# Kernel optimization log

Measured on AMD Instinct MI355X. Metric: run time of the kernel, lower is better.

The kernel has to match this reference:

```python
import jax, jax.numpy as jnp
import numpy as np

EMBED_DIM = 1024
N_HEADS = 16
KV_SIZE = 64
CLIP_DIST = 10
SLEN = 1024
BSZ = 8


def setup_inputs() -> dict:
    key = jax.random.key(0)
    ks = jax.random.split(key, 7)
    s = 0.02
    inputs = jax.random.normal(ks[0], (SLEN, BSZ, EMBED_DIM), dtype=jnp.float32)
    W_in = jax.random.normal(ks[1], (3 * N_HEADS * KV_SIZE, EMBED_DIM), dtype=jnp.float32) * s
    b_in = jnp.zeros((3 * N_HEADS * KV_SIZE,), dtype=jnp.float32)
    k_dist_emb = jax.random.normal(ks[2], (CLIP_DIST + 1, KV_SIZE), dtype=jnp.float32) * s
    v_dist_emb = jax.random.normal(ks[3], (CLIP_DIST + 1, KV_SIZE), dtype=jnp.float32) * s
    W_out = jax.random.normal(ks[4], (EMBED_DIM, N_HEADS * KV_SIZE), dtype=jnp.float32) * s
    b_out = jnp.zeros((EMBED_DIM,), dtype=jnp.float32)
    return {"inputs": inputs, "W_in": W_in, "b_in": b_in,
            "k_dist_emb": k_dist_emb, "v_dist_emb": v_dist_emb,
            "W_out": W_out, "b_out": b_out}


def reference(inputs, W_in, b_in, k_dist_emb, v_dist_emb, W_out, b_out):
    slen, bsz, _ = inputs.shape
    h, d = N_HEADS, KV_SIZE
    # in_proj: (slen, bsz, 3*h*d) -> (3, bsz, h, slen, d)
    qkv = inputs @ W_in.T + b_in
    qkv = qkv.reshape(slen, bsz, 3, h, d).transpose(2, 1, 3, 0, 4)
    q, k, v = qkv[0], qkv[1], qkv[2]
    q = q * (d ** -0.5)
    # clipped absolute relative distances (slen, slen)
    idx = jnp.arange(slen)
    dist = jnp.minimum(jnp.abs(idx[None, :] - idx[:, None]), CLIP_DIST)
    k_dist = k_dist_emb[dist]  # (slen, slen, d)
    v_dist = v_dist_emb[dist]  # (slen, slen, d)
    # content scores + relative-distance bias
    attn = jnp.einsum('bhsd,bhtd->bhst', q, k) + jnp.einsum('bhsd,std->bhst', q, k_dist)
    attn = jax.nn.softmax(attn, axis=-1)
    # value accumulation + relative-distance value correction
    out = jnp.einsum('bhst,bhtd->bhsd', attn, v) + jnp.einsum('bhst,std->bhsd', attn, v_dist)
    # (bsz, h, slen, d) -> (slen, bsz, h*d)
    out = out.transpose(2, 0, 1, 3).reshape(slen, bsz, h * d)
    return out @ W_out.T + b_out
```

## Files before the change

kernel.cpp:

```cpp
#include <hip/hip_runtime.h>
#include <hip/hip_bf16.h>
#include <cstdint>


typedef __attribute__((ext_vector_type(8))) __bf16 bf16x8;
typedef __attribute__((ext_vector_type(4))) __bf16 bf16x4;
typedef __attribute__((ext_vector_type(4))) short s16x4;
typedef __attribute__((ext_vector_type(4))) float f32x4;

#if __has_builtin(__builtin_amdgcn_exp2f)
#define EXP2F(x) __builtin_amdgcn_exp2f(x)
#else
#define EXP2F(x) exp2f(x)
#endif

#if __has_builtin(__builtin_amdgcn_mfma_f32_16x16x16bf16_1k)
#define PV_MFMA(ACC, AV, BV) \
  ACC = __builtin_amdgcn_mfma_f32_16x16x16bf16_1k( \
      __builtin_bit_cast(s16x4, AV), __builtin_bit_cast(s16x4, BV), ACC, 0, 0, 0)
#elif __has_builtin(__builtin_amdgcn_mfma_f32_16x16x16_bf16)
#define PV_MFMA(ACC, AV, BV) \
  ACC = __builtin_amdgcn_mfma_f32_16x16x16_bf16(AV, BV, ACC, 0, 0, 0)
#else
#define PV_MFMA(ACC, AV, BV)                                               \
  asm volatile("s_nop 1\n\tv_mfma_f32_16x16x16_bf16 %0, %1, %2, %0\n\t"    \
               "s_nop 7\n\ts_nop 7"                                        \
               : "+v"(ACC)                                                 \
               : "v"(__builtin_bit_cast(s16x4, AV)),                       \
                 "v"(__builtin_bit_cast(s16x4, BV)))
#endif

__device__ __forceinline__ void gload_lds16(const void* g, void* l) {
  __builtin_amdgcn_global_load_lds(
      (const __attribute__((address_space(1))) void*)g,
      (__attribute__((address_space(3))) void*)l, 16, 0, 0);
}

__global__ __launch_bounds__(256) void f2b3_kernel(
    const float* __restrict__ s0, __bf16* __restrict__ d0,
    const float* __restrict__ s1, __bf16* __restrict__ d1,
    const float* __restrict__ s2, __bf16* __restrict__ d2) {
  int i = (blockIdx.x * 256 + threadIdx.x) * 8;
  const float* s; __bf16* d; int off;
  if (i < 8388608) { s = s0; d = d0; off = i; }
  else if (i < 11534336) { s = s1; d = d1; off = i - 8388608; }
  else { s = s2; d = d2; off = i - 11534336; }
  float4 a = *(const float4*)(s + off);
  float4 b = *(const float4*)(s + off + 4);
  bf16x8 o;
  o[0] = (__bf16)a.x; o[1] = (__bf16)a.y; o[2] = (__bf16)a.z; o[3] = (__bf16)a.w;
  o[4] = (__bf16)b.x; o[5] = (__bf16)b.y; o[6] = (__bf16)b.z; o[7] = (__bf16)b.w;
  *(bf16x8*)(d + off) = o;
}


#define STG8A(SL, TK, G)                                                      \
  gload_lds16(A + (size_t)(m0 + (G) * 64 + (tid >> 3)) * K + (TK) * 64 + sgc, \
              (void*)&sG[SL][(G) * 4096 + wave * 512]);
#define STG8B(SL, TK, G)                                                      \
  gload_lds16(Bp + (size_t)(n0 + (G) * 64 + (tid >> 3)) * K + (TK) * 64 + sgc,\
              (void*)&sG[SL][16384 + (G) * 4096 + wave * 512]);

#define GPH(SL, MP, NP, STAGE_STMT, TAIL_STMT)                                  \
  {                                                                             \
    bf16x8 af[2][2], bfr[2][2];                                                 \
    _Pragma("unroll") for (int mi = 0; mi < 2; ++mi)                            \
      _Pragma("unroll") for (int kk = 0; kk < 2; ++kk)                          \
        af[mi][kk] = *(const bf16x8*)&sG[SL][                                   \
            (wr * 64 + ((MP) * 2 + mi) * 16 + lr) * 64 +                        \
            (((kk * 4 + lg) ^ (lr & 7)) * 8)];                                  \
    _Pragma("unroll") for (int ni = 0; ni < 2; ++ni)                            \
      _Pragma("unroll") for (int kk = 0; kk < 2; ++kk)                          \
        bfr[ni][kk] = *(const bf16x8*)&sG[SL][16384 +                           \
            (wc * 64 + ((NP) * 2 + ni) * 16 + lr) * 64 +                        \
            (((kk * 4 + lg) ^ (lr & 7)) * 8)];                                  \
    STAGE_STMT                                                                  \
    __builtin_amdgcn_s_barrier();                                               \
    asm volatile("s_waitcnt lgkmcnt(0)" ::: "memory");                          \
    __builtin_amdgcn_sched_barrier(0);                                          \
    __builtin_amdgcn_s_setprio(1);                                              \
    _Pragma("unroll") for (int mi = 0; mi < 2; ++mi)                            \
      _Pragma("unroll") for (int ni = 0; ni < 2; ++ni)                          \
        _Pragma("unroll") for (int kk = 0; kk < 2; ++kk)                        \
          acc[(MP) * 2 + mi][(NP) * 2 + ni] =                                   \
              __builtin_amdgcn_mfma_f32_16x16x32_bf16(                          \
                  af[mi][kk], bfr[ni][kk],                                      \
                  acc[(MP) * 2 + mi][(NP) * 2 + ni], 0, 0, 0);                  \
    __builtin_amdgcn_s_setprio(0);                                              \
    TAIL_STMT                                                                   \
    __builtin_amdgcn_s_barrier();                                               \
  }

#define GTILE(SL, SS, TK2, DOSTG, WAITC)                                        \
  GPH(SL, 0, 0, if (DOSTG) { STG8A(SS, TK2, 0) STG8A(SS, TK2, 1) }, )           \
  GPH(SL, 0, 1, if (DOSTG) { STG8A(SS, TK2, 2) STG8A(SS, TK2, 3) }, )           \
  GPH(SL, 1, 0, if (DOSTG) { STG8B(SS, TK2, 0) }, )                             \
  GPH(SL, 1, 1, if (DOSTG) { STG8B(SS, TK2, 1) },                               \
      if ((WAITC) == 6) { asm volatile("s_waitcnt vmcnt(6)" ::: "memory"); }    \
      else if ((WAITC) == 0) { asm volatile("s_waitcnt vmcnt(0)" ::: "memory"); })

template <int EPI>
__global__ __launch_bounds__(512) void gemm8p(
    const __bf16* __restrict__ A, const __bf16* __restrict__ Bp,
    const float* __restrict__ bias, int K,
    float* __restrict__ outF, __bf16* __restrict__ outT,
    __bf16* __restrict__ outV, int N, int NT, int CPX) {
  __shared__ __align__(16) __bf16 sG[3][24576];
  const int tid = threadIdx.x;
  const int wave = tid >> 6, lane = tid & 63;
  const int lg = lane >> 4, lr = lane & 15;
  const int wr = wave >> 1, wc = wave & 1;
  const int lid = (blockIdx.x & 7) * CPX + (blockIdx.x >> 3);
  const int m0 = (lid / NT) * 256;
  const int n0 = (lid % NT) * 128;

  const int sgc = ((tid & 7) ^ ((tid >> 3) & 7)) * 8;

  f32x4 acc[4][4] = {};

  STG8A(0, 0, 0) STG8A(0, 0, 1) STG8A(0, 0, 2) STG8A(0, 0, 3)
  STG8B(0, 0, 0) STG8B(0, 0, 1)
  STG8A(1, 1, 0) STG8A(1, 1, 1) STG8A(1, 1, 2) STG8A(1, 1, 3)
  STG8B(1, 1, 0) STG8B(1, 1, 1)
  asm volatile("s_waitcnt vmcnt(6)" ::: "memory");
  __builtin_amdgcn_s_barrier();

  GTILE(0, 2, 2, 1, 6)
  GTILE(1, 0, 3, 1, 6)
  GTILE(2, 1, 4, 1, 6)
  GTILE(0, 2, 5, 1, 6)
  GTILE(1, 0, 6, 1, 6)
  GTILE(2, 1, 7, 1, 6)
  GTILE(0, 2, 8, 1, 6)
  GTILE(1, 0, 9, 1, 6)
  GTILE(2, 1, 10, 1, 6)
  GTILE(0, 2, 11, 1, 6)
  GTILE(1, 0, 12, 1, 6)
  GTILE(2, 1, 13, 1, 6)
  GTILE(0, 2, 14, 1, 6)
  GTILE(1, 0, 15, 1, 6)
  GTILE(2, 1, 16, 0, 0)
  GTILE(0, 2, 17, 0, 2)

  if constexpr (EPI == 0) {
    const int tt = n0 >> 10;
    if (tt == 2) {
      __bf16* vtl = &sG[0][0];
#pragma unroll
      for (int mf = 0; mf < 4; ++mf) {
#pragma unroll
        for (int nf = 0; nf < 4; ++nf) {
          const int gn = n0 + wc * 64 + nf * 16 + lr;
          const float bv = bias[gn];
          const int d = nf * 16 + lr;
#pragma unroll
          for (int rg = 0; rg < 4; ++rg) {
            const int row = wr * 64 + mf * 16 + lg * 4 + rg;
            const float v = acc[mf][nf][rg] + bv;
            vtl[((size_t)((wc * 8 + (row & 7)) * 64 + d) << 5) + (row >> 3)] =
                (__bf16)v;
          }
        }
      }
      __syncthreads();
      const int s0g = m0 >> 3;
      const int hh = (n0 >> 6) & 15;
#pragma unroll
      for (int rr = 0; rr < 2; ++rr) {
        const int r = tid + rr * 512;
        const int hl = r >> 9, bb = (r >> 6) & 7, dd = r & 63;
        __bf16* dst = outV + ((size_t)((bb * 16 + hh + hl) * 64 + dd) << 10) + s0g;
        const __bf16* src = &vtl[(size_t)r << 5];
#pragma unroll
        for (int j = 0; j < 4; ++j)
          *(bf16x8*)&dst[j * 8] = *(const bf16x8*)&src[j * 8];
      }
      return;
    }
  }

#pragma unroll
  for (int mf = 0; mf < 4; ++mf) {
    const int gm0 = m0 + wr * 64 + mf * 16 + lg * 4;
#pragma unroll
    for (int nf = 0; nf < 4; ++nf) {
      const int gn = n0 + wc * 64 + nf * 16 + lr;
      const float bv = bias[gn];
#pragma unroll
      for (int rg = 0; rg < 4; ++rg) {
        const int gm = gm0 + rg;
        float v = acc[mf][nf][rg] + bv;
        if constexpr (EPI == 0) {
          int t = gn >> 10, h = (gn >> 6) & 15, d = gn & 63;
          int s = gm >> 3, b = gm & 7;
          if (t == 0) v *= 0.18033688011112042f;
          outT[(((size_t)((t * 8 + b) * 16 + h) * 1024 + s) << 6) + d] = (__bf16)v;
        } else {
          outF[(size_t)gm * N + gn] = v;
        }
      }
    }
  }
}

#define ATTN_TILE(KT, KC, KS, VC, VS)                                           \
  {                                                                             \
    if ((KT) < 15)                                                              \
      gload_lds16(vtp + (size_t)srow * 1024 + ((KT) + 1) * 64 + sc8,            \
                  &sV[VS][wave * 512]);                                         \
    if ((KT) < 14)                                                              \
      gload_lds16(kp + (size_t)((KT) * 64 + 128 + srow) * 64 + sc8,             \
                  &sK[KS][wave * 512]);                                         \
    f32x4 sf[4];                                                                \
    __builtin_amdgcn_s_setprio(1);                                              \
    _Pragma("unroll") for (int tj = 0; tj < 4; ++tj) {                          \
      const int t = tj * 16 + lr;                                               \
      bf16x8 bk0 = *(const bf16x8*)&sK[KC][t * 64 + ((lg ^ (t & 7)) * 8)];      \
      bf16x8 bk1 = *(const bf16x8*)&sK[KC][t * 64 + (((4 + lg) ^ (t & 7)) * 8)];\
      f32x4 z = {};                                                             \
      z = __builtin_amdgcn_mfma_f32_16x16x32_bf16(bk0, aq[0], z, 0, 0, 0);      \
      z = __builtin_amdgcn_mfma_f32_16x16x32_bf16(bk1, aq[1], z, 0, 0, 0);      \
      sf[tj] = z;                                                               \
    }                                                                           \
    __builtin_amdgcn_s_setprio(0);                                              \
    const bool inband = ((KT) * 64 <= sb + 24) && ((KT) * 64 + 63 >= sb - 9);   \
    if (inband) {                                                               \
      const float* bDrow = &sBD[wave][lr][0];                                   \
      _Pragma("unroll") for (int tj = 0; tj < 4; ++tj) {                        \
        _Pragma("unroll") for (int rg = 0; rg < 4; ++rg) {                      \
          const int t = (KT) * 64 + tj * 16 + lg * 4 + rg;                      \
          const int dd = t - s;                                                 \
          const int ad = dd < 0 ? -dd : dd;                                     \
          if (ad <= 9) {                                                        \
            const float val = sf[tj][rg] + bDrow[ad];                           \
            sf[tj][rg] = val;                                                   \
            band[wave][lr][dd + 9] = (__bf16)val;                               \
          }                                                                     \
        }                                                                       \
      }                                                                         \
    }                                                                           \
    float vm[4];                                                                \
    _Pragma("unroll") for (int tj = 0; tj < 4; ++tj)                            \
      vm[tj] = fmaxf(fmaxf(sf[tj][0], sf[tj][1]), fmaxf(sf[tj][2], sf[tj][3])); \
    float vmax = fmaxf(fmaxf(vm[0], vm[1]), fmaxf(vm[2], vm[3]));               \
    vmax = fmaxf(vmax, __shfl_xor(vmax, 16, 64));                               \
    vmax = fmaxf(vmax, __shfl_xor(vmax, 32, 64));                               \
    if (__any(vmax > m + 8.f)) {                                                \
      const float mn = fmaxf(m, vmax);                                          \
      const float scl = EXP2F(m - mn);                                          \
      m = mn;                                                                   \
      l *= scl;                                                                 \
      _Pragma("unroll") for (int dj = 0; dj < 4; ++dj)                          \
        _Pragma("unroll") for (int rg = 0; rg < 4; ++rg)                        \
          o_acc[dj][rg] *= scl;                                                 \
    }                                                                           \
    float rs[4];                                                                \
    _Pragma("unroll") for (int tj = 0; tj < 4; ++tj) {                          \
      float p0 = EXP2F(sf[tj][0] - m), p1 = EXP2F(sf[tj][1] - m);               \
      float p2 = EXP2F(sf[tj][2] - m), p3 = EXP2F(sf[tj][3] - m);               \
      sf[tj][0] = p0; sf[tj][1] = p1; sf[tj][2] = p2; sf[tj][3] = p3;           \
      rs[tj] = (p0 + p1) + (p2 + p3);                                           \
    }                                                                           \
    float rsum = (rs[0] + rs[1]) + (rs[2] + rs[3]);                             \
    rsum += __shfl_xor(rsum, 16, 64);                                           \
    rsum += __shfl_xor(rsum, 32, 64);                                           \
    l += rsum;                                                                  \
    bf16x4 pbv[4];                                                              \
    _Pragma("unroll") for (int tj = 0; tj < 4; ++tj) {                          \
      pbv[tj][0] = (__bf16)sf[tj][0]; pbv[tj][1] = (__bf16)sf[tj][1];           \
      pbv[tj][2] = (__bf16)sf[tj][2]; pbv[tj][3] = (__bf16)sf[tj][3];           \
    }                                                                           \
    __builtin_amdgcn_s_setprio(1);                                              \
    _Pragma("unroll") for (int tj = 0; tj < 4; ++tj) {                          \
      _Pragma("unroll") for (int dj = 0; dj < 4; ++dj) {                        \
        const int d = dj * 16 + lr;                                             \
        const int ch = (2 * tj + (lg >> 1)) ^ (d & 7);                          \
        const bf16x4 av = *(const bf16x4*)&sV[VC][d * 64 + ch * 8 + (lg & 1) * 4]; \
        PV_MFMA(o_acc[dj], av, pbv[tj]);                                        \
      }                                                                         \
    }                                                                           \
    __builtin_amdgcn_s_setprio(0);                                              \
    if ((KT) < 14) {                                                            \
      asm volatile("s_waitcnt vmcnt(1)" ::: "memory");                          \
    } else if ((KT) == 14) {                                                    \
      asm volatile("s_waitcnt vmcnt(0)" ::: "memory");                          \
    }                                                                           \
    if ((KT) < 15) __builtin_amdgcn_s_barrier();                                \
  }

__global__ __launch_bounds__(512) void attn_kernel(
    const __bf16* __restrict__ qkv, const __bf16* __restrict__ vt,
    const float* __restrict__ kde, const float* __restrict__ vde,
    __bf16* __restrict__ O) {
  __shared__ __align__(16) __bf16 sK[3][4096];
  __shared__ __align__(16) __bf16 sV[2][4096];
  __shared__ __bf16 band[8][16][20];
  __shared__ float sBD[8][16][10];
  const int tid = threadIdx.x, wave = tid >> 6, lane = tid & 63;
  const int lg = lane >> 4, lr = lane & 15;
  const int lid = (blockIdx.x & 7) * 128 + (blockIdx.x >> 3);
  const int bh = lid >> 3;
  const int stile = lid & 7;
  const int sb = stile * 128 + wave * 16;
  const int b = bh >> 4, h = bh & 15;
  const __bf16* qp = qkv + (size_t)bh * 65536;
  const __bf16* kp = qkv + (size_t)(128 + bh) * 65536;
  const __bf16* vtp = vt + (size_t)bh * 65536;

  const int srow = tid >> 3;
  const int sc8 = ((tid & 7) ^ (srow & 7)) * 8;

  gload_lds16(kp + (size_t)srow * 64 + sc8, &sK[0][wave * 512]);
  gload_lds16(vtp + (size_t)srow * 1024 + sc8, &sV[0][wave * 512]);
  gload_lds16(kp + (size_t)(64 + srow) * 64 + sc8, &sK[1][wave * 512]);

  {
    __bf16* bf = &band[0][0][0];
    for (int i = tid; i < 8 * 16 * 20; i += 512) bf[i] = (__bf16)(-1e30f);
  }

  bf16x8 aq[2];
#pragma unroll
  for (int kk = 0; kk < 2; ++kk)
    aq[kk] = *(const bf16x8*)&qp[(size_t)(sb + lr) * 64 + kk * 32 + lg * 8];

  {
    float kd10[16];
#pragma unroll
    for (int e = 0; e < 16; ++e)
      kd10[e] = kde[640 + (e >> 3) * 32 + lg * 8 + (e & 7)];
#pragma unroll
    for (int c = 0; c < 10; ++c) {
      float acc = 0.f;
#pragma unroll
      for (int e = 0; e < 16; ++e)
        acc += (float)aq[e >> 3][e & 7] *
               (kde[c * 64 + (e >> 3) * 32 + lg * 8 + (e & 7)] - kd10[e]);
      acc += __shfl_xor(acc, 16, 64);
      acc += __shfl_xor(acc, 32, 64);
      if (lg == 0) sBD[wave][lr][c] = acc;
    }
  }

  f32x4 o_acc[4] = {};
  float m = -1e30f, l = 0.f;
  const int s = sb + lr;

  asm volatile("s_waitcnt vmcnt(1)" ::: "memory");
  __builtin_amdgcn_s_barrier();

  ATTN_TILE( 0, 0, 2, 0, 1)
  ATTN_TILE( 1, 1, 0, 1, 0)
  ATTN_TILE( 2, 2, 1, 0, 1)
  ATTN_TILE( 3, 0, 2, 1, 0)
  ATTN_TILE( 4, 1, 0, 0, 1)
  ATTN_TILE( 5, 2, 1, 1, 0)
  ATTN_TILE( 6, 0, 2, 0, 1)
  ATTN_TILE( 7, 1, 0, 1, 0)
  ATTN_TILE( 8, 2, 1, 0, 1)
  ATTN_TILE( 9, 0, 2, 1, 0)
  ATTN_TILE(10, 1, 0, 0, 1)
  ATTN_TILE(11, 2, 1, 1, 0)
  ATTN_TILE(12, 0, 2, 0, 1)
  ATTN_TILE(13, 1, 0, 1, 0)
  ATTN_TILE(14, 2, 1, 0, 1)
  ATTN_TILE(15, 0, 2, 1, 0)

  const float inv = 1.f / l;
  float psum[10];
  psum[0] = EXP2F((float)band[wave][lr][9] - m);
#pragma unroll
  for (int c = 1; c < 10; ++c)
    psum[c] = EXP2F((float)band[wave][lr][9 - c] - m) +
              EXP2F((float)band[wave][lr][9 + c] - m);
#pragma unroll
  for (int dj = 0; dj < 4; ++dj) {
    bf16x4 ov;
#pragma unroll
    for (int rg = 0; rg < 4; ++rg) {
      const int d = dj * 16 + lg * 4 + rg;
      float acc2 = 0.f;
#pragma unroll
      for (int c = 0; c < 10; ++c)
        acc2 += psum[c] * (vde[c * 64 + d] - vde[640 + d]);
      ov[rg] = (__bf16)((o_acc[dj][rg] + acc2) * inv + vde[640 + d]);
    }
    *(bf16x4*)&O[((size_t)(s * 8 + b)) * 1024 + h * 64 + dj * 16 + lg * 4] = ov;
  }
}

extern "C" void kernel_launch(void* const* d_in, const int* in_sizes, int n_in,
                              void* d_out, int out_size, void* d_ws, size_t ws_size,
                              hipStream_t stream) {
  (void)in_sizes; (void)n_in; (void)out_size; (void)ws_size;
  const float* inputs = (const float*)d_in[0];
  const float* W_in   = (const float*)d_in[1];
  const float* b_in   = (const float*)d_in[2];
  const float* kde    = (const float*)d_in[3];
  const float* vde    = (const float*)d_in[4];
  const float* W_out  = (const float*)d_in[5];
  const float* b_out  = (const float*)d_in[6];
  float* out = (float*)d_out;

  char* ws = (char*)d_ws;
  __bf16* qkvt  = (__bf16*)(ws);
  __bf16* vt    = (__bf16*)(ws + 50331648);
  __bf16* Xb    = (__bf16*)(ws + 75497472);
  __bf16* Ob    = (__bf16*)(ws + 75497472);
  __bf16* Wb_in = (__bf16*)(ws + 92274688);
  __bf16* Wb_out= (__bf16*)(ws + 98566144);

  f2b3_kernel<<<6144, 256, 0, stream>>>(inputs, Xb, W_in, Wb_in, W_out, Wb_out);

  gemm8p<0><<<768, 512, 0, stream>>>(Xb, Wb_in, b_in, 1024, nullptr, qkvt, vt, 3072, 24, 96);
  attn_kernel<<<1024, 512, 0, stream>>>(qkvt, vt, kde, vde, Ob);
  gemm8p<1><<<256, 512, 0, stream>>>(Ob, Wb_out, b_out, 1024, out, nullptr, nullptr, 1024, 8, 32);
}
```

Before: 195.4 us.

## Process two 16-row query subtiles per wave in attention kernel

Each wave in the attention kernel now handles 32 query rows (two 16-row subtiles A and B) instead of 16, so each K/V tile staged in LDS is reused by twice as many MFMAs. The grid drops from 1024 to 512 blocks and each block covers 256 query rows, which halves the global K/V traffic and the LDS staging per query row. The cost is doubled accumulator and softmax state per wave, so register pressure rises and occupancy and parallelism fall, with only 512 blocks left on the GPU.

```diff
diff --git a/kernel.cpp b/kernel.cpp
--- a/kernel.cpp
+++ b/kernel.cpp
@@ -52,7 +52,6 @@
   o[4] = (__bf16)b.x; o[5] = (__bf16)b.y; o[6] = (__bf16)b.z; o[7] = (__bf16)b.w;
   *(bf16x8*)(d + off) = o;
 }
-
 
 #define STG8A(SL, TK, G)                                                      \
   gload_lds16(A + (size_t)(m0 + (G) * 64 + (tid >> 3)) * K + (TK) * 64 + sgc, \
@@ -211,64 +210,97 @@
     if ((KT) < 14)                                                              \
       gload_lds16(kp + (size_t)((KT) * 64 + 128 + srow) * 64 + sc8,             \
                   &sK[KS][wave * 512]);                                         \
-    f32x4 sf[4];                                                                \
+    f32x4 sfA[4], sfB[4];                                                       \
     __builtin_amdgcn_s_setprio(1);                                              \
     _Pragma("unroll") for (int tj = 0; tj < 4; ++tj) {                          \
       const int t = tj * 16 + lr;                                               \
       bf16x8 bk0 = *(const bf16x8*)&sK[KC][t * 64 + ((lg ^ (t & 7)) * 8)];      \
       bf16x8 bk1 = *(const bf16x8*)&sK[KC][t * 64 + (((4 + lg) ^ (t & 7)) * 8)];\
-      f32x4 z = {};                                                             \
-      z = __builtin_amdgcn_mfma_f32_16x16x32_bf16(bk0, aq[0], z, 0, 0, 0);      \
-      z = __builtin_amdgcn_mfma_f32_16x16x32_bf16(bk1, aq[1], z, 0, 0, 0);      \
-      sf[tj] = z;                                                               \
+      f32x4 zA = {}, zB = {};                                                   \
+      zA = __builtin_amdgcn_mfma_f32_16x16x32_bf16(bk0, aqA[0], zA, 0, 0, 0);   \
+      zA = __builtin_amdgcn_mfma_f32_16x16x32_bf16(bk1, aqA[1], zA, 0, 0, 0);   \
+      zB = __builtin_amdgcn_mfma_f32_16x16x32_bf16(bk0, aqB[0], zB, 0, 0, 0);   \
+      zB = __builtin_amdgcn_mfma_f32_16x16x32_bf16(bk1, aqB[1], zB, 0, 0, 0);   \
+      sfA[tj] = zA; sfB[tj] = zB;                                               \
     }                                                                           \
     __builtin_amdgcn_s_setprio(0);                                              \
-    const bool inband = ((KT) * 64 <= sb + 24) && ((KT) * 64 + 63 >= sb - 9);   \
+    const bool inband = ((KT) * 64 <= sb + 40) && ((KT) * 64 + 63 >= sb - 9);   \
     if (inband) {                                                               \
-      const float* bDrow = &sBD[wave][lr][0];                                   \
       _Pragma("unroll") for (int tj = 0; tj < 4; ++tj) {                        \
         _Pragma("unroll") for (int rg = 0; rg < 4; ++rg) {                      \
           const int t = (KT) * 64 + tj * 16 + lg * 4 + rg;                      \
-          const int dd = t - s;                                                 \
-          const int ad = dd < 0 ? -dd : dd;                                     \
-          if (ad <= 9) {                                                        \
-            const float val = sf[tj][rg] + bDrow[ad];                           \
-            sf[tj][rg] = val;                                                   \
-            band[wave][lr][dd + 9] = (__bf16)val;                               \
+          {                                                                     \
+            const int dd = t - sA;                                              \
+            const int ad = dd < 0 ? -dd : dd;                                   \
+            if (ad <= 9) {                                                      \
+              const float val = sfA[tj][rg] + sBD[wave][lr][ad];                \
+              sfA[tj][rg] = val;                                                \
+              band[wave][lr][dd + 9] = (__bf16)val;                             \
+            }                                                                   \
+          }                                                                     \
+          {                                                                     \
+            const int dd = t - sB2;                                             \
+            const int ad = dd < 0 ? -dd : dd;                                   \
+            if (ad <= 9) {                                                      \
+              const float val = sfB[tj][rg] + sBD[wave][16 + lr][ad];           \
+              sfB[tj][rg] = val;                                                \
+              band[wave][16 + lr][dd + 9] = (__bf16)val;                        \
+            }                                                                   \
           }                                                                     \
         }                                                                       \
       }                                                                         \
     }                                                                           \
-    float vm[4];                                                                \
-    _Pragma("unroll") for (int tj = 0; tj < 4; ++tj)                            \
-      vm[tj] = fmaxf(fmaxf(sf[tj][0], sf[tj][1]), fmaxf(sf[tj][2], sf[tj][3])); \
-    float vmax = fmaxf(fmaxf(vm[0], vm[1]), fmaxf(vm[2], vm[3]));               \
-    vmax = fmaxf(vmax, __shfl_xor(vmax, 16, 64));                               \
-    vmax = fmaxf(vmax, __shfl_xor(vmax, 32, 64));                               \
-    if (__any(vmax > m + 8.f)) {                                                \
-      const float mn = fmaxf(m, vmax);                                          \
-      const float scl = EXP2F(m - mn);                                          \
-      m = mn;                                                                   \
-      l *= scl;                                                                 \
-      _Pragma("unroll") for (int dj = 0; dj < 4; ++dj)                          \
-        _Pragma("unroll") for (int rg = 0; rg < 4; ++rg)                        \
-          o_acc[dj][rg] *= scl;                                                 \
-    }                                                                           \
-    float rs[4];                                                                \
-    _Pragma("unroll") for (int tj = 0; tj < 4; ++tj) {                          \
-      float p0 = EXP2F(sf[tj][0] - m), p1 = EXP2F(sf[tj][1] - m);               \
-      float p2 = EXP2F(sf[tj][2] - m), p3 = EXP2F(sf[tj][3] - m);               \
-      sf[tj][0] = p0; sf[tj][1] = p1; sf[tj][2] = p2; sf[tj][3] = p3;           \
-      rs[tj] = (p0 + p1) + (p2 + p3);                                           \
-    }                                                                           \
-    float rsum = (rs[0] + rs[1]) + (rs[2] + rs[3]);                             \
-    rsum += __shfl_xor(rsum, 16, 64);                                           \
-    rsum += __shfl_xor(rsum, 32, 64);                                           \
-    l += rsum;                                                                  \
-    bf16x4 pbv[4];                                                              \
-    _Pragma("unroll") for (int tj = 0; tj < 4; ++tj) {                          \
-      pbv[tj][0] = (__bf16)sf[tj][0]; pbv[tj][1] = (__bf16)sf[tj][1];           \
-      pbv[tj][2] = (__bf16)sf[tj][2]; pbv[tj][3] = (__bf16)sf[tj][3];           \
+    {                                                                           \
+      float vmA[4], vmB[4];                                                     \
+      _Pragma("unroll") for (int tj = 0; tj < 4; ++tj) {                        \
+        vmA[tj] = fmaxf(fmaxf(sfA[tj][0], sfA[tj][1]),                          \
+                        fmaxf(sfA[tj][2], sfA[tj][3]));                         \
+        vmB[tj] = fmaxf(fmaxf(sfB[tj][0], sfB[tj][1]),                          \
+                        fmaxf(sfB[tj][2], sfB[tj][3]));                         \
+      }                                                                         \
+      float vmaxA = fmaxf(fmaxf(vmA[0], vmA[1]), fmaxf(vmA[2], vmA[3]));        \
+      float vmaxB = fmaxf(fmaxf(vmB[0], vmB[1]), fmaxf(vmB[2], vmB[3]));        \
+      vmaxA = fmaxf(vmaxA, __shfl_xor(vmaxA, 16, 64));                          \
+      vmaxA = fmaxf(vmaxA, __shfl_xor(vmaxA, 32, 64));                          \
+      vmaxB = fmaxf(vmaxB, __shfl_xor(vmaxB, 16, 64));                          \
+      vmaxB = fmaxf(vmaxB, __shfl_xor(vmaxB, 32, 64));                          \
+      if (__any(vmaxA > mA + 8.f)) {                                            \
+        const float mn = fmaxf(mA, vmaxA);                                      \
+        const float scl = EXP2F(mA - mn);                                       \
+        mA = mn; lA *= scl;                                                     \
+        _Pragma("unroll") for (int dj = 0; dj < 4; ++dj)                        \
+          _Pragma("unroll") for (int rg = 0; rg < 4; ++rg)                      \
+            o_accA[dj][rg] *= scl;                                              \
+      }                                                                         \
+      if (__any(vmaxB > mB + 8.f)) {                                            \
+        const float mn = fmaxf(mB, vmaxB);                                      \
+        const float scl = EXP2F(mB - mn);                                       \
+        mB = mn; lB *= scl;                                                     \
+        _Pragma("unroll") for (int dj = 0; dj < 4; ++dj)                        \
+          _Pragma("unroll") for (int rg = 0; rg < 4; ++rg)                      \
+            o_accB[dj][rg] *= scl;                                              \
+      }                                                                         \
+    }                                                                           \
+    bf16x4 pbvA[4], pbvB[4];                                                    \
+    {                                                                           \
+      float rsA = 0.f, rsB = 0.f;                                               \
+      _Pragma("unroll") for (int tj = 0; tj < 4; ++tj) {                        \
+        float a0 = EXP2F(sfA[tj][0] - mA), a1 = EXP2F(sfA[tj][1] - mA);         \
+        float a2 = EXP2F(sfA[tj][2] - mA), a3 = EXP2F(sfA[tj][3] - mA);         \
+        rsA += (a0 + a1) + (a2 + a3);                                           \
+        pbvA[tj][0] = (__bf16)a0; pbvA[tj][1] = (__bf16)a1;                     \
+        pbvA[tj][2] = (__bf16)a2; pbvA[tj][3] = (__bf16)a3;                     \
+        float b0 = EXP2F(sfB[tj][0] - mB), b1 = EXP2F(sfB[tj][1] - mB);         \
+        float b2 = EXP2F(sfB[tj][2] - mB), b3 = EXP2F(sfB[tj][3] - mB);         \
+        rsB += (b0 + b1) + (b2 + b3);                                           \
+        pbvB[tj][0] = (__bf16)b0; pbvB[tj][1] = (__bf16)b1;                     \
+        pbvB[tj][2] = (__bf16)b2; pbvB[tj][3] = (__bf16)b3;                     \
+      }                                                                         \
+      rsA += __shfl_xor(rsA, 16, 64);                                           \
+      rsA += __shfl_xor(rsA, 32, 64);                                           \
+      rsB += __shfl_xor(rsB, 16, 64);                                           \
+      rsB += __shfl_xor(rsB, 32, 64);                                           \
+      lA += rsA; lB += rsB;                                                     \
     }                                                                           \
     __builtin_amdgcn_s_setprio(1);                                              \
     _Pragma("unroll") for (int tj = 0; tj < 4; ++tj) {                          \
@@ -276,7 +308,8 @@
         const int d = dj * 16 + lr;                                             \
         const int ch = (2 * tj + (lg >> 1)) ^ (d & 7);                          \
         const bf16x4 av = *(const bf16x4*)&sV[VC][d * 64 + ch * 8 + (lg & 1) * 4]; \
-        PV_MFMA(o_acc[dj], av, pbv[tj]);                                        \
+        PV_MFMA(o_accA[dj], av, pbvA[tj]);                                      \
+        PV_MFMA(o_accB[dj], av, pbvB[tj]);                                      \
       }                                                                         \
     }                                                                           \
     __builtin_amdgcn_s_setprio(0);                                              \
@@ -294,14 +327,14 @@
     __bf16* __restrict__ O) {
   __shared__ __align__(16) __bf16 sK[3][4096];
   __shared__ __align__(16) __bf16 sV[2][4096];
-  __shared__ __bf16 band[8][16][20];
-  __shared__ float sBD[8][16][10];
+  __shared__ __bf16 band[8][32][20];
+  __shared__ float sBD[8][32][10];
   const int tid = threadIdx.x, wave = tid >> 6, lane = tid & 63;
   const int lg = lane >> 4, lr = lane & 15;
-  const int lid = (blockIdx.x & 7) * 128 + (blockIdx.x >> 3);
-  const int bh = lid >> 3;
-  const int stile = lid & 7;
-  const int sb = stile * 128 + wave * 16;
+  const int lid = (blockIdx.x & 7) * 64 + (blockIdx.x >> 3);
+  const int bh = lid >> 2;
+  const int stile = lid & 3;
+  const int sb = stile * 256 + wave * 32;
   const int b = bh >> 4, h = bh & 15;
   const __bf16* qp = qkv + (size_t)bh * 65536;
   const __bf16* kp = qkv + (size_t)(128 + bh) * 65536;
@@ -316,13 +349,15 @@
 
   {
     __bf16* bf = &band[0][0][0];
-    for (int i = tid; i < 8 * 16 * 20; i += 512) bf[i] = (__bf16)(-1e30f);
-  }
-
-  bf16x8 aq[2];
-#pragma unroll
-  for (int kk = 0; kk < 2; ++kk)
-    aq[kk] = *(const bf16x8*)&qp[(size_t)(sb + lr) * 64 + kk * 32 + lg * 8];
+    for (int i = tid; i < 8 * 32 * 20; i += 512) bf[i] = (__bf16)(-1e30f);
+  }
+
+  bf16x8 aqA[2], aqB[2];
+#pragma unroll
+  for (int kk = 0; kk < 2; ++kk) {
+    aqA[kk] = *(const bf16x8*)&qp[(size_t)(sb + lr) * 64 + kk * 32 + lg * 8];
+    aqB[kk] = *(const bf16x8*)&qp[(size_t)(sb + 16 + lr) * 64 + kk * 32 + lg * 8];
+  }
 
   {
     float kd10[16];
@@ -331,20 +366,28 @@
       kd10[e] = kde[640 + (e >> 3) * 32 + lg * 8 + (e & 7)];
 #pragma unroll
     for (int c = 0; c < 10; ++c) {
-      float acc = 0.f;
-#pragma unroll
-      for (int e = 0; e < 16; ++e)
-        acc += (float)aq[e >> 3][e & 7] *
-               (kde[c * 64 + (e >> 3) * 32 + lg * 8 + (e & 7)] - kd10[e]);
-      acc += __shfl_xor(acc, 16, 64);
-      acc += __shfl_xor(acc, 32, 64);
-      if (lg == 0) sBD[wave][lr][c] = acc;
+      float accA = 0.f, accB = 0.f;
+#pragma unroll
+      for (int e = 0; e < 16; ++e) {
+        const float kd = kde[c * 64 + (e >> 3) * 32 + lg * 8 + (e & 7)] - kd10[e];
+        accA += (float)aqA[e >> 3][e & 7] * kd;
+        accB += (float)aqB[e >> 3][e & 7] * kd;
+      }
+      accA += __shfl_xor(accA, 16, 64);
+      accA += __shfl_xor(accA, 32, 64);
+      accB += __shfl_xor(accB, 16, 64);
+      accB += __shfl_xor(accB, 32, 64);
+      if (lg == 0) {
+        sBD[wave][lr][c] = accA;
+        sBD[wave][16 + lr][c] = accB;
+      }
     }
   }
 
-  f32x4 o_acc[4] = {};
-  float m = -1e30f, l = 0.f;
-  const int s = sb + lr;
+  f32x4 o_accA[4] = {}, o_accB[4] = {};
+  float mA = -1e30f, lA = 0.f, mB = -1e30f, lB = 0.f;
+  const int sA = sb + lr;
+  const int sB2 = sb + 16 + lr;
 
   asm volatile("s_waitcnt vmcnt(1)" ::: "memory");
   __builtin_amdgcn_s_barrier();
@@ -366,26 +409,33 @@
   ATTN_TILE(14, 2, 1, 0, 1)
   ATTN_TILE(15, 0, 2, 1, 0)
 
-  const float inv = 1.f / l;
-  float psum[10];
-  psum[0] = EXP2F((float)band[wave][lr][9] - m);
-#pragma unroll
-  for (int c = 1; c < 10; ++c)
-    psum[c] = EXP2F((float)band[wave][lr][9 - c] - m) +
-              EXP2F((float)band[wave][lr][9 + c] - m);
-#pragma unroll
-  for (int dj = 0; dj < 4; ++dj) {
-    bf16x4 ov;
-#pragma unroll
-    for (int rg = 0; rg < 4; ++rg) {
-      const int d = dj * 16 + lg * 4 + rg;
-      float acc2 = 0.f;
-#pragma unroll
-      for (int c = 0; c < 10; ++c)
-        acc2 += psum[c] * (vde[c * 64 + d] - vde[640 + d]);
-      ov[rg] = (__bf16)((o_acc[dj][rg] + acc2) * inv + vde[640 + d]);
+#pragma unroll
+  for (int sub = 0; sub < 2; ++sub) {
+    const int sr = sub ? sB2 : sA;
+    const int br = sub ? 16 + lr : lr;
+    const float mm = sub ? mB : mA;
+    const float inv = 1.f / (sub ? lB : lA);
+    const f32x4* oa = sub ? o_accB : o_accA;
+    float psum[10];
+    psum[0] = EXP2F((float)band[wave][br][9] - mm);
+#pragma unroll
+    for (int c = 1; c < 10; ++c)
+      psum[c] = EXP2F((float)band[wave][br][9 - c] - mm) +
+                EXP2F((float)band[wave][br][9 + c] - mm);
+#pragma unroll
+    for (int dj = 0; dj < 4; ++dj) {
+      bf16x4 ov;
+#pragma unroll
+      for (int rg = 0; rg < 4; ++rg) {
+        const int d = dj * 16 + lg * 4 + rg;
+        float acc2 = 0.f;
+#pragma unroll
+        for (int c = 0; c < 10; ++c)
+          acc2 += psum[c] * (vde[c * 64 + d] - vde[640 + d]);
+        ov[rg] = (__bf16)((oa[dj][rg] + acc2) * inv + vde[640 + d]);
+      }
+      *(bf16x4*)&O[((size_t)(sr * 8 + b)) * 1024 + h * 64 + dj * 16 + lg * 4] = ov;
     }
-    *(bf16x4*)&O[((size_t)(s * 8 + b)) * 1024 + h * 64 + dj * 16 + lg * 4] = ov;
   }
 }
 
@@ -413,6 +463,6 @@
   f2b3_kernel<<<6144, 256, 0, stream>>>(inputs, Xb, W_in, Wb_in, W_out, Wb_out);
 
   gemm8p<0><<<768, 512, 0, stream>>>(Xb, Wb_in, b_in, 1024, nullptr, qkvt, vt, 3072, 24, 96);
-  attn_kernel<<<1024, 512, 0, stream>>>(qkvt, vt, kde, vde, Ob);
+  attn_kernel<<<512, 512, 0, stream>>>(qkvt, vt, kde, vde, Ob);
   gemm8p<1><<<256, 512, 0, stream>>>(Ob, Wb_out, b_out, 1024, out, nullptr, nullptr, 1024, 8, 32);
 }
```

Result: slower. 220.7 us (+13.0%).
